# Performance work log

Measured on AMD Instinct MI355X. Metric: run time of the kernel, lower is better.

The kernel has to match this reference:

```python
import jax, jax.numpy as jnp
import numpy as np

V, F = 100000, 200000
N, H, W, K = 4, 512, 512, 8
SHININESS = 64.0
SIGMA, GAMMA = 1e-4, 1e-4
ZNEAR, ZFAR, EPS = 1.0, 100.0, 1e-10
BACKGROUND = (1.0, 1.0, 1.0)

def _normalize(x, axis=-1):
    return x / jnp.maximum(jnp.linalg.norm(x, axis=axis, keepdims=True), 1e-6)

def setup_inputs() -> dict:
    key = jax.random.key(0)
    ks = jax.random.split(key, 13)
    verts = jax.random.normal(ks[0], (V, 3), jnp.float32)
    normals = _normalize(jax.random.normal(ks[1], (V, 3), jnp.float32))
    vertex_colors = jax.random.uniform(ks[2], (V, 3), jnp.float32)
    faces = jax.random.randint(ks[3], (F, 3), 0, V, jnp.int32)
    # include background pixels: values in [-1, F-1)
    pix_to_face = jax.random.randint(ks[4], (N, H, W, K), 0, F, jnp.int32) - 1
    bary = jax.random.uniform(ks[5], (N, H, W, K, 3), jnp.float32) + 1e-3
    bary_coords = bary / bary.sum(-1, keepdims=True)
    dists = jax.random.normal(ks[6], (N, H, W, K), jnp.float32) * (2.0 * SIGMA)
    zbuf = ZNEAR + jax.random.uniform(ks[7], (N, H, W, K), jnp.float32) * (ZFAR - ZNEAR)
    light_pos = jax.random.normal(ks[8], (3,), jnp.float32) * 3.0
    camera_pos = jax.random.normal(ks[9], (3,), jnp.float32) * 3.0
    ambient_color = jax.random.uniform(ks[10], (3,), jnp.float32) * 0.5
    diffuse_color = jax.random.uniform(ks[11], (3,), jnp.float32)
    specular_color = jax.random.uniform(ks[12], (3,), jnp.float32) * 0.3
    return dict(verts=verts, normals=normals, vertex_colors=vertex_colors,
                faces=faces, pix_to_face=pix_to_face, bary_coords=bary_coords,
                dists=dists, zbuf=zbuf, light_pos=light_pos, camera_pos=camera_pos,
                ambient_color=ambient_color, diffuse_color=diffuse_color,
                specular_color=specular_color)

def reference(verts, normals, vertex_colors, faces, pix_to_face, bary_coords,
              dists, zbuf, light_pos, camera_pos, ambient_color, diffuse_color,
              specular_color):
    # --- per-vertex Phong lighting (gouraud_shading) ---
    n = _normalize(normals)
    ldir = _normalize(light_pos[None, :] - verts)            # (V,3)
    vdir = _normalize(camera_pos[None, :] - verts)           # (V,3)
    cos_l = jax.nn.relu(jnp.sum(n * ldir, -1, keepdims=True))
    diffuse = diffuse_color[None, :] * cos_l                  # (V,3)
    refl = -ldir + 2.0 * jnp.sum(ldir * n, -1, keepdims=True) * n
    cos_s = jax.nn.relu(jnp.sum(refl * vdir, -1, keepdims=True))
    specular = specular_color[None, :] * cos_s ** SHININESS   # (V,3)
    vcol = vertex_colors * (ambient_color[None, :] + diffuse) + specular  # (V,3)
    # --- barycentric interpolation of per-vertex colors ---
    face_colors = vcol[faces]                                  # (F,3,3)
    mask = pix_to_face >= 0                                    # (N,H,W,K)
    p2f = jnp.where(mask, pix_to_face, 0)
    gathered = face_colors[p2f]                                # (N,H,W,K,3,3)
    colors = jnp.einsum('nhwkv,nhwkvc->nhwkc', bary_coords, gathered)
    # --- softmax_rgb_blend ---
    maskf = mask.astype(colors.dtype)
    prob = jax.nn.sigmoid(-dists / SIGMA) * maskf              # (N,H,W,K)
    alpha = 1.0 - jnp.prod(1.0 - prob, axis=-1)                # (N,H,W)
    z_inv = (ZFAR - zbuf) / (ZFAR - ZNEAR) * maskf
    z_inv_max = jnp.maximum(z_inv.max(-1, keepdims=True), EPS) # (N,H,W,1)
    w_num = prob * jnp.exp((z_inv - z_inv_max) / GAMMA)        # (N,H,W,K)
    delta = jnp.exp((EPS - z_inv_max[..., 0]) / GAMMA)         # (N,H,W)
    denom = w_num.sum(-1) + delta                              # (N,H,W)
    wcol = jnp.einsum('nhwk,nhwkc->nhwc', w_num, colors) / denom[..., None]
    bg = jnp.asarray(BACKGROUND, colors.dtype)
    rgb = wcol + (delta / denom)[..., None] * bg[None, None, None, :]
    return jnp.concatenate([rgb, alpha[..., None]], axis=-1)   # (N,H,W,4)
```

## Files before the change

### kernel.cpp

```cpp
#include <hip/hip_runtime.h>
#include <math.h>

constexpr float SIGMA  = 1e-4f;
constexpr float GAMMA  = 1e-4f;
constexpr float ZNEAR  = 1.0f;
constexpr float ZFAR   = 100.0f;
constexpr float EPSV   = 1e-10f;
constexpr int   KK     = 8;

constexpr float LOG2E    = 1.4426950408889634f;
constexpr float ISIG_L2E = LOG2E / SIGMA;
constexpr float IGAM_L2E = LOG2E / GAMMA;
constexpr float INV_ZR   = 1.0f / (ZFAR - ZNEAR);
constexpr float ARG_CUT  = -100.0f;

typedef unsigned int u32;
typedef float f32x4 __attribute__((ext_vector_type(4)));
typedef int   i32x4 __attribute__((ext_vector_type(4)));
typedef u32   u32x4 __attribute__((ext_vector_type(4)));

extern "C" __device__ float __builtin_amdgcn_exp2f(float);
extern "C" __device__ float __builtin_amdgcn_rcpf(float);

constexpr float INV11 = 2.0f / 2047.0f;
constexpr float INV10 = 2.0f / 1023.0f;

__device__ inline u32 pack_rgb(float r, float g, float b) {
    u32 qr = (u32)(fminf(fmaxf(r, 0.0f), 2.0f) * (2047.0f / 2.0f) + 0.5f);
    u32 qg = (u32)(fminf(fmaxf(g, 0.0f), 2.0f) * (2047.0f / 2.0f) + 0.5f);
    u32 qb = (u32)(fminf(fmaxf(b, 0.0f), 2.0f) * (1023.0f / 2.0f) + 0.5f);
    return qr | (qg << 11) | (qb << 22);
}

__device__ inline void accum_color(u32x4 gv, float b0, float b1, float b2,
                                   float w, float& wr, float& wg, float& wb) {
    float r = b0 * (float)(gv[0] & 0x7FFu)
            + b1 * (float)(gv[1] & 0x7FFu)
            + b2 * (float)(gv[2] & 0x7FFu);
    float g = b0 * (float)((gv[0] >> 11) & 0x7FFu)
            + b1 * (float)((gv[1] >> 11) & 0x7FFu)
            + b2 * (float)((gv[2] >> 11) & 0x7FFu);
    float b = b0 * (float)(gv[0] >> 22)
            + b1 * (float)(gv[1] >> 22)
            + b2 * (float)(gv[2] >> 22);
    wr += w * (r * INV11);
    wg += w * (g * INV11);
    wb += w * (b * INV10);
}

__global__ __launch_bounds__(256) void vertex_shade_kernel(
    const float* __restrict__ verts,
    const float* __restrict__ normals,
    const float* __restrict__ vertex_colors,
    const float* __restrict__ light_pos,
    const float* __restrict__ camera_pos,
    const float* __restrict__ ambient_color,
    const float* __restrict__ diffuse_color,
    const float* __restrict__ specular_color,
    f32x4* __restrict__ vcol4, int V)
{
    int v = blockIdx.x * blockDim.x + threadIdx.x;
    if (v >= V) return;

    float px = verts[3*v+0], py = verts[3*v+1], pz = verts[3*v+2];
    float nx = normals[3*v+0], ny = normals[3*v+1], nz = normals[3*v+2];

    float nn = fmaxf(sqrtf(nx*nx + ny*ny + nz*nz), 1e-6f);
    nx /= nn; ny /= nn; nz /= nn;

    float lx = light_pos[0] - px, ly = light_pos[1] - py, lz = light_pos[2] - pz;
    float ln = fmaxf(sqrtf(lx*lx + ly*ly + lz*lz), 1e-6f);
    lx /= ln; ly /= ln; lz /= ln;

    float vx = camera_pos[0] - px, vy = camera_pos[1] - py, vz = camera_pos[2] - pz;
    float vn = fmaxf(sqrtf(vx*vx + vy*vy + vz*vz), 1e-6f);
    vx /= vn; vy /= vn; vz /= vn;

    float dot_ln = nx*lx + ny*ly + nz*lz;
    float cos_l = fmaxf(dot_ln, 0.0f);

    float rx = -lx + 2.0f * dot_ln * nx;
    float ry = -ly + 2.0f * dot_ln * ny;
    float rz = -lz + 2.0f * dot_ln * nz;
    float cos_s = fmaxf(rx*vx + ry*vy + rz*vz, 0.0f);

    float s = cos_s;
    s = s*s; s = s*s; s = s*s; s = s*s; s = s*s; s = s*s;

    f32x4 o;
    o[0] = vertex_colors[3*v+0] * (ambient_color[0] + diffuse_color[0] * cos_l) + specular_color[0] * s;
    o[1] = vertex_colors[3*v+1] * (ambient_color[1] + diffuse_color[1] * cos_l) + specular_color[1] * s;
    o[2] = vertex_colors[3*v+2] * (ambient_color[2] + diffuse_color[2] * cos_l) + specular_color[2] * s;
    o[3] = 0.0f;
    vcol4[v] = o;
}

__global__ __launch_bounds__(256) void build_face_colors_kernel(
    const int*  __restrict__ faces,
    const f32x4* __restrict__ vcol4,
    u32x4* __restrict__ fc,
    int F)
{
    int f = blockIdx.x * blockDim.x + threadIdx.x;
    if (f >= F) return;
    int i0 = faces[3*f+0], i1 = faces[3*f+1], i2 = faces[3*f+2];
    f32x4 c0 = vcol4[i0], c1 = vcol4[i1], c2 = vcol4[i2];
    u32x4 a;
    a[0] = pack_rgb(c0[0], c0[1], c0[2]);
    a[1] = pack_rgb(c1[0], c1[1], c1[2]);
    a[2] = pack_rgb(c2[0], c2[1], c2[2]);
    a[3] = 0u;
    fc[f] = a;
}

__global__ __launch_bounds__(256) void pixel_blend_fc_kernel(
    const i32x4* __restrict__ p2f4,
    const float* __restrict__ bary,
    const f32x4* __restrict__ d4,
    const f32x4* __restrict__ z4,
    const u32x4* __restrict__ fc,
    f32x4* __restrict__ out,
    int npix)
{
    int pix = blockIdx.x * blockDim.x + threadIdx.x;
    if (pix >= npix) return;

    i32x4 fA = p2f4[2*pix + 0];
    i32x4 fB = p2f4[2*pix + 1];
    f32x4 dA = d4[2*pix + 0];
    f32x4 dB = d4[2*pix + 1];
    f32x4 zA = z4[2*pix + 0];
    f32x4 zB = z4[2*pix + 1];

    int   fidx[KK] = {fA[0], fA[1], fA[2], fA[3], fB[0], fB[1], fB[2], fB[3]};
    float dd[KK]   = {dA[0], dA[1], dA[2], dA[3], dB[0], dB[1], dB[2], dB[3]};
    float zz[KK]   = {zA[0], zA[1], zA[2], zA[3], zB[0], zB[1], zB[2], zB[3]};

    float prob[KK], zinv[KK];
    float zmax = EPSV;
    float one_minus = 1.0f;

    #pragma unroll
    for (int k = 0; k < KK; ++k) {
        bool m = fidx[k] >= 0;
        float e  = __builtin_amdgcn_exp2f(dd[k] * ISIG_L2E);
        float pr = m ? __builtin_amdgcn_rcpf(1.0f + e) : 0.0f;
        prob[k] = pr;
        one_minus *= (1.0f - pr);

        float zi = m ? (ZFAR - zz[k]) * INV_ZR : 0.0f;
        zinv[k] = zi;
        zmax = fmaxf(zmax, zi);
    }

    int kbest = 0;
    float zb = zinv[0];
    #pragma unroll
    for (int k = 1; k < KK; ++k) {
        bool gt = zinv[k] > zb;
        zb    = gt ? zinv[k] : zb;
        kbest = gt ? k : kbest;
    }

    int fb = fidx[kbest] < 0 ? 0 : fidx[kbest];
    u32x4 gv = fc[fb];
    const float* bp_base = bary + (size_t)pix * (KK*3);
    const float* bp = bp_base + 3*kbest;
    float b0 = bp[0], b1 = bp[1], b2 = bp[2];

    float w[KK];
    float denom = 0.0f;
    #pragma unroll
    for (int k = 0; k < KK; ++k) {
        float arg = (zinv[k] - zmax) * IGAM_L2E;
        w[k] = prob[k] * __builtin_amdgcn_exp2f(arg);
        denom += w[k];
    }

    float wr = 0.0f, wg = 0.0f, wb = 0.0f;
    accum_color(gv, b0, b1, b2, w[kbest], wr, wg, wb);

    #pragma unroll
    for (int k = 0; k < KK; ++k) {
        float arg = (zinv[k] - zmax) * IGAM_L2E;
        bool extra = (k != kbest) && (arg > ARG_CUT) && (prob[k] != 0.0f);
        if (extra) {
            u32x4 ge = fc[fidx[k]];
            const float* bpe = bp_base + 3*k;
            accum_color(ge, bpe[0], bpe[1], bpe[2], w[k], wr, wg, wb);
        }
    }

    float delta = __builtin_amdgcn_exp2f((EPSV - zmax) * IGAM_L2E);
    denom += delta;
    float inv = __builtin_amdgcn_rcpf(denom);

    f32x4 o;
    o[0] = (wr + delta) * inv;
    o[1] = (wg + delta) * inv;
    o[2] = (wb + delta) * inv;
    o[3] = 1.0f - one_minus;
    __builtin_nontemporal_store(o, out + pix);
}

__global__ __launch_bounds__(256) void pixel_blend_v4_kernel(
    const i32x4* __restrict__ p2f4,
    const f32x4* __restrict__ bary4,
    const f32x4* __restrict__ d4,
    const f32x4* __restrict__ z4,
    const int*   __restrict__ faces,
    const f32x4* __restrict__ vcol4,
    f32x4* __restrict__ out,
    int npix)
{
    int pix = blockIdx.x * blockDim.x + threadIdx.x;
    if (pix >= npix) return;

    i32x4 fA = p2f4[2*pix + 0];
    i32x4 fB = p2f4[2*pix + 1];
    int fidx[KK] = {fA[0], fA[1], fA[2], fA[3], fB[0], fB[1], fB[2], fB[3]};

    f32x4 dA = d4[2*pix + 0];
    f32x4 dB = d4[2*pix + 1];
    float dd[KK] = {dA[0], dA[1], dA[2], dA[3], dB[0], dB[1], dB[2], dB[3]};

    f32x4 zA = z4[2*pix + 0];
    f32x4 zB = z4[2*pix + 1];
    float zz[KK] = {zA[0], zA[1], zA[2], zA[3], zB[0], zB[1], zB[2], zB[3]};

    float bb[KK*3];
    #pragma unroll
    for (int i = 0; i < 6; ++i) {
        f32x4 t = bary4[6*(size_t)pix + i];
        bb[4*i+0] = t[0]; bb[4*i+1] = t[1]; bb[4*i+2] = t[2]; bb[4*i+3] = t[3];
    }

    int vi[KK][3];
    #pragma unroll
    for (int k = 0; k < KK; ++k) {
        int f = fidx[k] < 0 ? 0 : fidx[k];
        vi[k][0] = faces[3*f+0];
        vi[k][1] = faces[3*f+1];
        vi[k][2] = faces[3*f+2];
    }

    float prob[KK], zinv[KK];
    float colr[KK], colg[KK], colb[KK];
    float zmax = EPSV;
    float one_minus = 1.0f;

    #pragma unroll
    for (int k = 0; k < KK; ++k) {
        bool m = fidx[k] >= 0;
        float sig = 1.0f / (1.0f + expf(dd[k] / SIGMA));
        float pr = m ? sig : 0.0f;
        prob[k] = pr;
        one_minus *= (1.0f - pr);

        float zi = m ? (ZFAR - zz[k]) / (ZFAR - ZNEAR) : 0.0f;
        zinv[k] = zi;
        zmax = fmaxf(zmax, zi);

        f32x4 c0 = vcol4[vi[k][0]];
        f32x4 c1 = vcol4[vi[k][1]];
        f32x4 c2 = vcol4[vi[k][2]];
        float b0 = bb[3*k+0], b1 = bb[3*k+1], b2 = bb[3*k+2];
        colr[k] = b0*c0[0] + b1*c1[0] + b2*c2[0];
        colg[k] = b0*c0[1] + b1*c1[1] + b2*c2[1];
        colb[k] = b0*c0[2] + b1*c1[2] + b2*c2[2];
    }

    float denom = 0.0f, wr = 0.0f, wg = 0.0f, wb = 0.0f;
    #pragma unroll
    for (int k = 0; k < KK; ++k) {
        float w = prob[k] * expf((zinv[k] - zmax) / GAMMA);
        denom += w;
        wr += w * colr[k];
        wg += w * colg[k];
        wb += w * colb[k];
    }
    float delta = expf((EPSV - zmax) / GAMMA);
    denom += delta;
    float inv = 1.0f / denom;

    f32x4 o;
    o[0] = wr * inv + delta * inv;
    o[1] = wg * inv + delta * inv;
    o[2] = wb * inv + delta * inv;
    o[3] = 1.0f - one_minus;
    __builtin_nontemporal_store(o, out + pix);
}

extern "C" void kernel_launch(void* const* d_in, const int* in_sizes, int n_in,
                              void* d_out, int out_size, void* d_ws, size_t ws_size,
                              hipStream_t stream)
{
    const float* verts          = (const float*)d_in[0];
    const float* normals        = (const float*)d_in[1];
    const float* vertex_colors  = (const float*)d_in[2];
    const int*   faces          = (const int*)d_in[3];
    const int*   pix_to_face    = (const int*)d_in[4];
    const float* bary_coords    = (const float*)d_in[5];
    const float* dists          = (const float*)d_in[6];
    const float* zbuf           = (const float*)d_in[7];
    const float* light_pos      = (const float*)d_in[8];
    const float* camera_pos     = (const float*)d_in[9];
    const float* ambient_color  = (const float*)d_in[10];
    const float* diffuse_color  = (const float*)d_in[11];
    const float* specular_color = (const float*)d_in[12];

    int V    = in_sizes[0] / 3;
    int F    = in_sizes[3] / 3;
    int npix = in_sizes[4] / KK;

    size_t fc_bytes    = (size_t)F * 16;
    size_t vcol4_bytes = (size_t)V * 16;
    bool fast = ws_size >= fc_bytes + vcol4_bytes;

    if (fast) {
        u32x4* fc    = (u32x4*)d_ws;
        f32x4* vcol4 = (f32x4*)((char*)d_ws + fc_bytes);

        vertex_shade_kernel<<<(V + 255) / 256, 256, 0, stream>>>(
            verts, normals, vertex_colors, light_pos, camera_pos,
            ambient_color, diffuse_color, specular_color, vcol4, V);

        build_face_colors_kernel<<<(F + 255) / 256, 256, 0, stream>>>(
            faces, vcol4, fc, F);

        pixel_blend_fc_kernel<<<(npix + 255) / 256, 256, 0, stream>>>(
            (const i32x4*)pix_to_face, bary_coords,
            (const f32x4*)dists, (const f32x4*)zbuf,
            fc, (f32x4*)d_out, npix);
    } else {
        f32x4* vcol4 = (f32x4*)d_ws;

        vertex_shade_kernel<<<(V + 255) / 256, 256, 0, stream>>>(
            verts, normals, vertex_colors, light_pos, camera_pos,
            ambient_color, diffuse_color, specular_color, vcol4, V);

        pixel_blend_v4_kernel<<<(npix + 255) / 256, 256, 0, stream>>>(
            (const i32x4*)pix_to_face, (const f32x4*)bary_coords,
            (const f32x4*)dists, (const f32x4*)zbuf,
            faces, vcol4, (f32x4*)d_out, npix);
    }
}
```

Before: 60.53 us.

## Map one thread per pixel sample and reduce across lanes with shuffles

The pixel blend kernel now assigns one thread to each (pixel, k) sample instead of one thread per pixel. Each thread computes its own probability, inverse depth and face-color contribution, and the max, product and sums over the 8 samples are formed with xor shuffles. This gives fully coalesced scalar loads of pix_to_face, dists, zbuf and bary, and eight times more threads to hide the latency of the random face-color gathers. In exchange it adds shuffle overhead, and only one lane in eight does the output store. It also unconditionally gathers every eligible sample's face color, dropping the old special case for the best sample.

```diff
diff --git a/kernel.cpp b/kernel.cpp
--- a/kernel.cpp
+++ b/kernel.cpp
@@ -30,22 +30,6 @@
     u32 qg = (u32)(fminf(fmaxf(g, 0.0f), 2.0f) * (2047.0f / 2.0f) + 0.5f);
     u32 qb = (u32)(fminf(fmaxf(b, 0.0f), 2.0f) * (1023.0f / 2.0f) + 0.5f);
     return qr | (qg << 11) | (qb << 22);
-}
-
-__device__ inline void accum_color(u32x4 gv, float b0, float b1, float b2,
-                                   float w, float& wr, float& wg, float& wb) {
-    float r = b0 * (float)(gv[0] & 0x7FFu)
-            + b1 * (float)(gv[1] & 0x7FFu)
-            + b2 * (float)(gv[2] & 0x7FFu);
-    float g = b0 * (float)((gv[0] >> 11) & 0x7FFu)
-            + b1 * (float)((gv[1] >> 11) & 0x7FFu)
-            + b2 * (float)((gv[2] >> 11) & 0x7FFu);
-    float b = b0 * (float)(gv[0] >> 22)
-            + b1 * (float)(gv[1] >> 22)
-            + b2 * (float)(gv[2] >> 22);
-    wr += w * (r * INV11);
-    wg += w * (g * INV11);
-    wb += w * (b * INV10);
 }
 
 __global__ __launch_bounds__(256) void vertex_shade_kernel(
@@ -113,94 +97,80 @@
     fc[f] = a;
 }
 
-__global__ __launch_bounds__(256) void pixel_blend_fc_kernel(
-    const i32x4* __restrict__ p2f4,
+__global__ __launch_bounds__(256) void pixel_blend_tr_kernel(
+    const int*   __restrict__ p2f,
     const float* __restrict__ bary,
-    const f32x4* __restrict__ d4,
-    const f32x4* __restrict__ z4,
+    const float* __restrict__ dists,
+    const float* __restrict__ zbuf,
     const u32x4* __restrict__ fc,
     f32x4* __restrict__ out,
-    int npix)
-{
-    int pix = blockIdx.x * blockDim.x + threadIdx.x;
-    if (pix >= npix) return;
-
-    i32x4 fA = p2f4[2*pix + 0];
-    i32x4 fB = p2f4[2*pix + 1];
-    f32x4 dA = d4[2*pix + 0];
-    f32x4 dB = d4[2*pix + 1];
-    f32x4 zA = z4[2*pix + 0];
-    f32x4 zB = z4[2*pix + 1];
-
-    int   fidx[KK] = {fA[0], fA[1], fA[2], fA[3], fB[0], fB[1], fB[2], fB[3]};
-    float dd[KK]   = {dA[0], dA[1], dA[2], dA[3], dB[0], dB[1], dB[2], dB[3]};
-    float zz[KK]   = {zA[0], zA[1], zA[2], zA[3], zB[0], zB[1], zB[2], zB[3]};
-
-    float prob[KK], zinv[KK];
-    float zmax = EPSV;
-    float one_minus = 1.0f;
-
-    #pragma unroll
-    for (int k = 0; k < KK; ++k) {
-        bool m = fidx[k] >= 0;
-        float e  = __builtin_amdgcn_exp2f(dd[k] * ISIG_L2E);
-        float pr = m ? __builtin_amdgcn_rcpf(1.0f + e) : 0.0f;
-        prob[k] = pr;
-        one_minus *= (1.0f - pr);
-
-        float zi = m ? (ZFAR - zz[k]) * INV_ZR : 0.0f;
-        zinv[k] = zi;
-        zmax = fmaxf(zmax, zi);
-    }
-
-    int kbest = 0;
-    float zb = zinv[0];
-    #pragma unroll
-    for (int k = 1; k < KK; ++k) {
-        bool gt = zinv[k] > zb;
-        zb    = gt ? zinv[k] : zb;
-        kbest = gt ? k : kbest;
-    }
-
-    int fb = fidx[kbest] < 0 ? 0 : fidx[kbest];
-    u32x4 gv = fc[fb];
-    const float* bp_base = bary + (size_t)pix * (KK*3);
-    const float* bp = bp_base + 3*kbest;
+    int nsamp)
+{
+    int tid = blockIdx.x * blockDim.x + threadIdx.x;
+    if (tid >= nsamp) return;
+    int pix = tid >> 3;
+    int k   = tid & 7;
+    (void)k;
+
+    int   f  = p2f[tid];
+    float dd = dists[tid];
+    float zz = zbuf[tid];
+    const float* bp = bary + 3*(size_t)tid;
     float b0 = bp[0], b1 = bp[1], b2 = bp[2];
 
-    float w[KK];
-    float denom = 0.0f;
-    #pragma unroll
-    for (int k = 0; k < KK; ++k) {
-        float arg = (zinv[k] - zmax) * IGAM_L2E;
-        w[k] = prob[k] * __builtin_amdgcn_exp2f(arg);
-        denom += w[k];
-    }
-
-    float wr = 0.0f, wg = 0.0f, wb = 0.0f;
-    accum_color(gv, b0, b1, b2, w[kbest], wr, wg, wb);
-
-    #pragma unroll
-    for (int k = 0; k < KK; ++k) {
-        float arg = (zinv[k] - zmax) * IGAM_L2E;
-        bool extra = (k != kbest) && (arg > ARG_CUT) && (prob[k] != 0.0f);
-        if (extra) {
-            u32x4 ge = fc[fidx[k]];
-            const float* bpe = bp_base + 3*k;
-            accum_color(ge, bpe[0], bpe[1], bpe[2], w[k], wr, wg, wb);
-        }
-    }
-
-    float delta = __builtin_amdgcn_exp2f((EPSV - zmax) * IGAM_L2E);
-    denom += delta;
-    float inv = __builtin_amdgcn_rcpf(denom);
-
-    f32x4 o;
-    o[0] = (wr + delta) * inv;
-    o[1] = (wg + delta) * inv;
-    o[2] = (wb + delta) * inv;
-    o[3] = 1.0f - one_minus;
-    __builtin_nontemporal_store(o, out + pix);
+    bool  m  = f >= 0;
+    float e  = __builtin_amdgcn_exp2f(dd * ISIG_L2E);
+    float pr = m ? __builtin_amdgcn_rcpf(1.0f + e) : 0.0f;
+    float zi = m ? (ZFAR - zz) * INV_ZR : 0.0f;
+
+    float zmax = fmaxf(zi, EPSV);
+    zmax = fmaxf(zmax, __shfl_xor(zmax, 1));
+    zmax = fmaxf(zmax, __shfl_xor(zmax, 2));
+    zmax = fmaxf(zmax, __shfl_xor(zmax, 4));
+
+    float om = 1.0f - pr;
+    om *= __shfl_xor(om, 1);
+    om *= __shfl_xor(om, 2);
+    om *= __shfl_xor(om, 4);
+
+    float arg = (zi - zmax) * IGAM_L2E;
+    float w   = pr * __builtin_amdgcn_exp2f(arg);
+    float cr = 0.0f, cg = 0.0f, cb = 0.0f;
+    if (arg > ARG_CUT && pr != 0.0f) {
+        u32x4 gv = fc[f];
+        float r = b0 * (float)(gv[0] & 0x7FFu)
+                + b1 * (float)(gv[1] & 0x7FFu)
+                + b2 * (float)(gv[2] & 0x7FFu);
+        float g = b0 * (float)((gv[0] >> 11) & 0x7FFu)
+                + b1 * (float)((gv[1] >> 11) & 0x7FFu)
+                + b2 * (float)((gv[2] >> 11) & 0x7FFu);
+        float b = b0 * (float)(gv[0] >> 22)
+                + b1 * (float)(gv[1] >> 22)
+                + b2 * (float)(gv[2] >> 22);
+        cr = w * (r * INV11);
+        cg = w * (g * INV11);
+        cb = w * (b * INV10);
+    }
+
+    float ws = w;
+    #pragma unroll
+    for (int mask = 1; mask <= 4; mask <<= 1) {
+        ws += __shfl_xor(ws, mask);
+        cr += __shfl_xor(cr, mask);
+        cg += __shfl_xor(cg, mask);
+        cb += __shfl_xor(cb, mask);
+    }
+
+    if ((tid & 7) == 0) {
+        float delta = __builtin_amdgcn_exp2f((EPSV - zmax) * IGAM_L2E);
+        float inv   = __builtin_amdgcn_rcpf(ws + delta);
+        f32x4 o;
+        o[0] = (cr + delta) * inv;
+        o[1] = (cg + delta) * inv;
+        o[2] = (cb + delta) * inv;
+        o[3] = 1.0f - om;
+        __builtin_nontemporal_store(o, out + pix);
+    }
 }
 
 __global__ __launch_bounds__(256) void pixel_blend_v4_kernel(
@@ -309,9 +279,10 @@
     const float* diffuse_color  = (const float*)d_in[11];
     const float* specular_color = (const float*)d_in[12];
 
-    int V    = in_sizes[0] / 3;
-    int F    = in_sizes[3] / 3;
-    int npix = in_sizes[4] / KK;
+    int V     = in_sizes[0] / 3;
+    int F     = in_sizes[3] / 3;
+    int nsamp = in_sizes[4];
+    int npix  = nsamp / KK;
 
     size_t fc_bytes    = (size_t)F * 16;
     size_t vcol4_bytes = (size_t)V * 16;
@@ -328,10 +299,9 @@
         build_face_colors_kernel<<<(F + 255) / 256, 256, 0, stream>>>(
             faces, vcol4, fc, F);
 
-        pixel_blend_fc_kernel<<<(npix + 255) / 256, 256, 0, stream>>>(
-            (const i32x4*)pix_to_face, bary_coords,
-            (const f32x4*)dists, (const f32x4*)zbuf,
-            fc, (f32x4*)d_out, npix);
+        pixel_blend_tr_kernel<<<(nsamp + 255) / 256, 256, 0, stream>>>(
+            pix_to_face, bary_coords, dists, zbuf,
+            fc, (f32x4*)d_out, nsamp);
     } else {
         f32x4* vcol4 = (f32x4*)d_ws;
 
```

Result: slower. 61.89 us (+2.2%).
